# Kernel tuning notes

Hardware: AMD Instinct MI355X
Metric: run time of the kernel (lower is better)

## Reference

```python
import jax, jax.numpy as jnp
import numpy as np

NEG_SLOPE = 0.2
EPS = 1e-16


def _add_self_loops(edge_index, num_nodes):
    loop = jnp.arange(num_nodes, dtype=edge_index.dtype)
    return jnp.concatenate([edge_index, jnp.stack([loop, loop])], axis=1)


def gat_conv(x, edge_index, W, a_src, a_dst, b, concat):
    """PyG-style GATConv: gather -> attention logits -> segment softmax -> scatter-add."""
    N = x.shape[0]
    H, C = a_src.shape
    xl = (x @ W).reshape(N, H, C)                       # [N,H,C]
    alpha_src = (xl * a_src[None]).sum(-1)              # [N,H]
    alpha_dst = (xl * a_dst[None]).sum(-1)              # [N,H]
    src, dst = edge_index[0], edge_index[1]
    alpha = jax.nn.leaky_relu(alpha_src[src] + alpha_dst[dst], NEG_SLOPE)  # [E,H]
    amax = jax.ops.segment_max(alpha, dst, num_segments=N)
    amax = jnp.where(jnp.isfinite(amax), amax, 0.0)
    ea = jnp.exp(alpha - amax[dst])
    denom = jax.ops.segment_sum(ea, dst, num_segments=N)
    attn = ea / (denom[dst] + EPS)                      # [E,H]
    msg = xl[src] * attn[:, :, None]                    # [E,H,C]
    out = jax.ops.segment_sum(msg, dst, num_segments=N)  # [N,H,C]
    out = out.reshape(N, H * C) if concat else out.mean(axis=1)
    return out + b


def setup_inputs() -> dict:
    key = jax.random.key(0)
    ks = jax.random.split(key, 9)
    N, F, E, H, C, NC = 100000, 128, 1600000, 8, 8, 40
    s = lambda fan: 1.0 / np.sqrt(fan)
    return {
        "x": jax.random.normal(ks[0], (N, F), dtype=jnp.float32),
        "edge_index": jax.random.randint(ks[1], (2, E), 0, N, dtype=jnp.int64),
        "W1": jax.random.normal(ks[2], (F, H * C), dtype=jnp.float32) * s(F),
        "a_src1": jax.random.normal(ks[3], (H, C), dtype=jnp.float32) * s(C),
        "a_dst1": jax.random.normal(ks[4], (H, C), dtype=jnp.float32) * s(C),
        "b1": jnp.zeros((H * C,), dtype=jnp.float32),
        "W2": jax.random.normal(ks[5], (H * C, NC), dtype=jnp.float32) * s(H * C),
        "a_src2": jax.random.normal(ks[6], (1, NC), dtype=jnp.float32) * s(NC),
        "a_dst2": jax.random.normal(ks[7], (1, NC), dtype=jnp.float32) * s(NC),
        "b2": jnp.zeros((NC,), dtype=jnp.float32),
    }


def reference(x, edge_index, W1, a_src1, a_dst1, b1, W2, a_src2, a_dst2, b2):
    N = x.shape[0]
    ei = _add_self_loops(edge_index, N)
    h = gat_conv(x, ei, W1, a_src1, a_dst1, b1, concat=True)   # [N,64]
    h = jax.nn.elu(h)
    out = gat_conv(h, ei, W2, a_src2, a_dst2, b2, concat=True)  # [N,nclass]
    return out
```

## Files before the change

### kernel.cpp

```cpp
#include <hip/hip_runtime.h>
#include <math.h>

#define NEG_SLOPE 0.2f
#define GAT_EPS 1e-16f

#define CH   8192
#define NBK  256

__device__ __forceinline__ unsigned pack_bf16(float a, float b) {
    unsigned ua = __float_as_uint(a);
    unsigned ub = __float_as_uint(b);
    ua = (ua + 0x8000u) >> 16;
    ub = (ub + 0x8000u) & 0xffff0000u;
    return ua | ub;
}
__device__ __forceinline__ float bf_lo(unsigned pk) {
    return __uint_as_float(pk << 16);
}
__device__ __forceinline__ float bf_hi(unsigned pk) {
    return __uint_as_float(pk & 0xffff0000u);
}


__global__ __launch_bounds__(256) void k_cnt(
    const int* __restrict__ ei, int E, int N, int shift,
    int* __restrict__ cnt)
{
    __shared__ int h[NBK];
    int c = blockIdx.x;
    h[threadIdx.x] = 0;
    __syncthreads();
    int Etot = E + N;
    int base = c * CH;
    int lim = min(base + CH, Etot);
    for (int e = base + threadIdx.x; e < lim; e += 256) {
        int d = (e < E) ? ei[E + e] : (e - E);
        atomicAdd(&h[d >> shift], 1);
    }
    __syncthreads();
    cnt[c * NBK + threadIdx.x] = h[threadIdx.x];
}

__global__ __launch_bounds__(256) void k_off_a(
    const int* __restrict__ cnt, int* __restrict__ off,
    int* __restrict__ tot, int NCH)
{
    __shared__ int sm[256];
    int b = blockIdx.x;
    int t = threadIdx.x;
    int carry = 0;
    for (int c0 = 0; c0 < NCH; c0 += 256) {
        int c = c0 + t;
        int v = (c < NCH) ? cnt[c * NBK + b] : 0;
        sm[t] = v;
        __syncthreads();
        for (int o = 1; o < 256; o <<= 1) {
            int add = (t >= o) ? sm[t - o] : 0;
            __syncthreads();
            sm[t] += add;
            __syncthreads();
        }
        if (c < NCH) off[c * NBK + b] = carry + sm[t] - v;
        carry += sm[255];
        __syncthreads();
    }
    if (t == 0) tot[b] = carry;
}

__global__ __launch_bounds__(256) void k_off_b(
    const int* __restrict__ tot, int* __restrict__ bbase)
{
    __shared__ int sm[NBK];
    int b = threadIdx.x;
    int v0 = tot[b];
    sm[b] = v0;
    __syncthreads();
    for (int o = 1; o < NBK; o <<= 1) {
        int v = (b >= o) ? sm[b - o] : 0;
        __syncthreads();
        sm[b] += v;
        __syncthreads();
    }
    bbase[b] = sm[b] - v0;
    if (b == NBK - 1) bbase[NBK] = sm[b];
}

__global__ __launch_bounds__(256) void k_place(
    const int* __restrict__ ei, int E, int N, int shift,
    const int* __restrict__ off, const int* __restrict__ bbase,
    unsigned* __restrict__ bslab)
{
    __shared__ int cur[NBK];
    int c = blockIdx.x;
    cur[threadIdx.x] = bbase[threadIdx.x] + off[c * NBK + threadIdx.x];
    __syncthreads();
    int Etot = E + N;
    int base = c * CH;
    int lim = min(base + CH, Etot);
    int mask = (1 << shift) - 1;
    for (int e = base + threadIdx.x; e < lim; e += 256) {
        int s, d;
        if (e < E) { s = ei[e]; d = ei[E + e]; }
        else       { s = e - E; d = s; }
        int b = d >> shift;
        int pos = atomicAdd(&cur[b], 1);
        bslab[pos] = (unsigned)s | ((unsigned)(d & mask) << 17);
    }
}

__global__ __launch_bounds__(256) void k_csr2(
    const int* __restrict__ bbase, const unsigned* __restrict__ bslab,
    int shift, int* __restrict__ row_ptr, int* __restrict__ csr_src,
    int N, int Etot)
{
    __shared__ int sdeg[1024];
    __shared__ int scur[1024];
    __shared__ int ps[256];
    int b = blockIdx.x;
    int tid = threadIdx.x;
    int beg = bbase[b], end = bbase[b + 1];
    int nodes = 1 << shift;
    int node0 = b << shift;
    for (int i = tid; i < nodes; i += 256) sdeg[i] = 0;
    __syncthreads();
    for (int i = beg + tid; i < end; i += 256)
        atomicAdd(&sdeg[bslab[i] >> 17], 1);
    __syncthreads();
    int per = (nodes + 255) / 256;
    int mybase = tid * per;
    int sum = 0;
    for (int j = 0; j < per; j++) sum += sdeg[mybase + j];
    ps[tid] = sum;
    __syncthreads();
    int v0 = ps[tid];
    for (int o = 1; o < 256; o <<= 1) {
        int v = (tid >= o) ? ps[tid - o] : 0;
        __syncthreads();
        ps[tid] += v;
        __syncthreads();
    }
    int run = ps[tid] - v0;
    for (int j = 0; j < per; j++) {
        int i = mybase + j;
        int dgi = sdeg[i];
        scur[i] = beg + run;
        int node = node0 + i;
        if (node < N) row_ptr[node] = beg + run;
        run += dgi;
    }
    if (b == 0 && tid == 0) row_ptr[N] = Etot;
    __syncthreads();
    for (int i = beg + tid; i < end; i += 256) {
        unsigned w = bslab[i];
        int pos = atomicAdd(&scur[w >> 17], 1);
        csr_src[pos] = (int)(w & 0x1FFFFu);
    }
}

__global__ __launch_bounds__(256) void k_gemm1(
    const float* __restrict__ x, const float* __restrict__ W1,
    const float* __restrict__ a_src1, const float* __restrict__ a_dst1,
    unsigned* __restrict__ xl1b, float* __restrict__ as1,
    float* __restrict__ ad1, int N, int F)
{
    __shared__ float Ws[128 * 64];
    __shared__ float asrc[64];
    __shared__ float adst[64];
    for (int i = threadIdx.x; i < F * 64; i += 256) Ws[i] = W1[i];
    if (threadIdx.x < 64) {
        asrc[threadIdx.x] = a_src1[threadIdx.x];
        adst[threadIdx.x] = a_dst1[threadIdx.x];
    }
    __syncthreads();

    int n = blockIdx.x * 64 + (threadIdx.x >> 2);
    int q = threadIdx.x & 3;
    if (n >= N) return;
    int c0 = q * 16;

    float acc[16];
#pragma unroll
    for (int c = 0; c < 16; c++) acc[c] = 0.0f;

    const float4* xr4 = (const float4*)(x + (size_t)n * F);
    for (int k4 = 0; k4 < F / 4; k4++) {
        float4 xv = xr4[k4];
        const float* w0 = &Ws[(k4 * 4 + 0) * 64 + c0];
        const float* w1 = &Ws[(k4 * 4 + 1) * 64 + c0];
        const float* w2 = &Ws[(k4 * 4 + 2) * 64 + c0];
        const float* w3 = &Ws[(k4 * 4 + 3) * 64 + c0];
#pragma unroll
        for (int c = 0; c < 16; c++) {
            float a = acc[c];
            a = fmaf(xv.x, w0[c], a);
            a = fmaf(xv.y, w1[c], a);
            a = fmaf(xv.z, w2[c], a);
            a = fmaf(xv.w, w3[c], a);
            acc[c] = a;
        }
    }

    uint4 pk0, pk1;
    pk0.x = pack_bf16(acc[0], acc[1]);  pk0.y = pack_bf16(acc[2], acc[3]);
    pk0.z = pack_bf16(acc[4], acc[5]);  pk0.w = pack_bf16(acc[6], acc[7]);
    pk1.x = pack_bf16(acc[8], acc[9]);  pk1.y = pack_bf16(acc[10], acc[11]);
    pk1.z = pack_bf16(acc[12], acc[13]); pk1.w = pack_bf16(acc[14], acc[15]);
    uint4* xo = (uint4*)(xl1b + (size_t)n * 32 + q * 8);
    xo[0] = pk0;
    xo[1] = pk1;

#pragma unroll
    for (int hh = 0; hh < 2; hh++) {
        float s = 0.0f, t = 0.0f;
#pragma unroll
        for (int c = 0; c < 8; c++) {
            s = fmaf(acc[hh * 8 + c], asrc[c0 + hh * 8 + c], s);
            t = fmaf(acc[hh * 8 + c], adst[c0 + hh * 8 + c], t);
        }
        as1[(size_t)n * 8 + 2 * q + hh] = s;
        ad1[(size_t)n * 8 + 2 * q + hh] = t;
    }
}

__global__ __launch_bounds__(256) void k_agg1(
    const int* __restrict__ row_ptr, const int* __restrict__ csr_src,
    const float* __restrict__ as1, const float* __restrict__ ad1,
    const unsigned* __restrict__ xl1b, const float* __restrict__ b1,
    float* __restrict__ h1, int N)
{
    int d = blockIdx.x * 4 + (threadIdx.x >> 6);
    int lane = threadIdx.x & 63;
    if (d >= N) return;
    int g = lane >> 3;
    int l = lane & 7;

    int beg = row_ptr[d], end = row_ptr[d + 1];
    float adh = ad1[(size_t)d * 8 + l];

    float ax[8];
#pragma unroll
    for (int j = 0; j < 8; j++) ax[j] = 0.f;
    float den = 0.f;

    int i = beg + g;
    for (; i + 8 < end; i += 16) {
        int s0 = csr_src[i];
        int s1 = csr_src[i + 8];
        float al0 = as1[(size_t)s0 * 8 + l] + adh;
        float al1 = as1[(size_t)s1 * 8 + l] + adh;
        uint4 k0 = *(const uint4*)(xl1b + (size_t)s0 * 32 + l * 4);
        uint4 k1 = *(const uint4*)(xl1b + (size_t)s1 * 32 + l * 4);
        al0 = al0 > 0.f ? al0 : NEG_SLOPE * al0;
        al1 = al1 > 0.f ? al1 : NEG_SLOPE * al1;
        float e0 = __expf(al0);
        float e1 = __expf(al1);
        ax[0] = fmaf(e0, bf_lo(k0.x), ax[0]);
        ax[1] = fmaf(e0, bf_hi(k0.x), ax[1]);
        ax[2] = fmaf(e0, bf_lo(k0.y), ax[2]);
        ax[3] = fmaf(e0, bf_hi(k0.y), ax[3]);
        ax[4] = fmaf(e0, bf_lo(k0.z), ax[4]);
        ax[5] = fmaf(e0, bf_hi(k0.z), ax[5]);
        ax[6] = fmaf(e0, bf_lo(k0.w), ax[6]);
        ax[7] = fmaf(e0, bf_hi(k0.w), ax[7]);
        ax[0] = fmaf(e1, bf_lo(k1.x), ax[0]);
        ax[1] = fmaf(e1, bf_hi(k1.x), ax[1]);
        ax[2] = fmaf(e1, bf_lo(k1.y), ax[2]);
        ax[3] = fmaf(e1, bf_hi(k1.y), ax[3]);
        ax[4] = fmaf(e1, bf_lo(k1.z), ax[4]);
        ax[5] = fmaf(e1, bf_hi(k1.z), ax[5]);
        ax[6] = fmaf(e1, bf_lo(k1.w), ax[6]);
        ax[7] = fmaf(e1, bf_hi(k1.w), ax[7]);
        den += e0 + e1;
    }
    if (i < end) {
        int s0 = csr_src[i];
        float al0 = as1[(size_t)s0 * 8 + l] + adh;
        uint4 k0 = *(const uint4*)(xl1b + (size_t)s0 * 32 + l * 4);
        al0 = al0 > 0.f ? al0 : NEG_SLOPE * al0;
        float e0 = __expf(al0);
        ax[0] = fmaf(e0, bf_lo(k0.x), ax[0]);
        ax[1] = fmaf(e0, bf_hi(k0.x), ax[1]);
        ax[2] = fmaf(e0, bf_lo(k0.y), ax[2]);
        ax[3] = fmaf(e0, bf_hi(k0.y), ax[3]);
        ax[4] = fmaf(e0, bf_lo(k0.z), ax[4]);
        ax[5] = fmaf(e0, bf_hi(k0.z), ax[5]);
        ax[6] = fmaf(e0, bf_lo(k0.w), ax[6]);
        ax[7] = fmaf(e0, bf_hi(k0.w), ax[7]);
        den += e0;
    }

#pragma unroll
    for (int m = 8; m < 64; m <<= 1) {
#pragma unroll
        for (int j = 0; j < 8; j++) ax[j] += __shfl_xor(ax[j], m);
        den += __shfl_xor(den, m);
    }

    if (g == 0) {
        float inv = 1.f / (den + GAT_EPS);
        const float4* bb = (const float4*)(b1 + l * 8);
        float4 b0 = bb[0], b1v = bb[1];
        float4 o0, o1;
        float v;
        v = ax[0] * inv + b0.x; o0.x = v > 0.f ? v : expm1f(v);
        v = ax[1] * inv + b0.y; o0.y = v > 0.f ? v : expm1f(v);
        v = ax[2] * inv + b0.z; o0.z = v > 0.f ? v : expm1f(v);
        v = ax[3] * inv + b0.w; o0.w = v > 0.f ? v : expm1f(v);
        v = ax[4] * inv + b1v.x; o1.x = v > 0.f ? v : expm1f(v);
        v = ax[5] * inv + b1v.y; o1.y = v > 0.f ? v : expm1f(v);
        v = ax[6] * inv + b1v.z; o1.z = v > 0.f ? v : expm1f(v);
        v = ax[7] * inv + b1v.w; o1.w = v > 0.f ? v : expm1f(v);
        float4* op = (float4*)(h1 + (size_t)d * 64 + l * 8);
        op[0] = o0;
        op[1] = o1;
    }
}

__global__ __launch_bounds__(256) void k_node2(
    const float* __restrict__ h1, const float* __restrict__ W2,
    const float* __restrict__ a_src2, const float* __restrict__ a_dst2,
    unsigned* __restrict__ xl2b, float* __restrict__ as2,
    float* __restrict__ ad2, int N)
{
    __shared__ float Ws[64 * 40];
    __shared__ float a2s[40];
    __shared__ float a2d[40];
    for (int i = threadIdx.x; i < 64 * 40; i += 256) Ws[i] = W2[i];
    if (threadIdx.x < 40) {
        a2s[threadIdx.x] = a_src2[threadIdx.x];
        a2d[threadIdx.x] = a_dst2[threadIdx.x];
    }
    __syncthreads();

    int n = blockIdx.x * 128 + (threadIdx.x >> 1);
    int q = threadIdx.x & 1;
    if (n >= N) return;
    int c0 = q * 20;

    float o[20];
#pragma unroll
    for (int j = 0; j < 20; j++) o[j] = 0.0f;

    const float4* hr4 = (const float4*)(h1 + (size_t)n * 64);
    for (int k4 = 0; k4 < 16; k4++) {
        float4 hv = hr4[k4];
        const float* w0 = &Ws[(k4 * 4 + 0) * 40 + c0];
        const float* w1 = &Ws[(k4 * 4 + 1) * 40 + c0];
        const float* w2 = &Ws[(k4 * 4 + 2) * 40 + c0];
        const float* w3 = &Ws[(k4 * 4 + 3) * 40 + c0];
#pragma unroll
        for (int j = 0; j < 20; j++) {
            float a = o[j];
            a = fmaf(hv.x, w0[j], a);
            a = fmaf(hv.y, w1[j], a);
            a = fmaf(hv.z, w2[j], a);
            a = fmaf(hv.w, w3[j], a);
            o[j] = a;
        }
    }

    float s = 0.0f, t = 0.0f;
#pragma unroll
    for (int j = 0; j < 20; j++) {
        s = fmaf(o[j], a2s[c0 + j], s);
        t = fmaf(o[j], a2d[c0 + j], t);
    }
    s += __shfl_xor(s, 1);
    t += __shfl_xor(t, 1);
    if (q == 0) { as2[n] = s; ad2[n] = t; }

    unsigned* xo = xl2b + (size_t)n * 20 + q * 10;
#pragma unroll
    for (int p = 0; p < 10; p++) xo[p] = pack_bf16(o[2 * p], o[2 * p + 1]);
}

__global__ __launch_bounds__(256) void k_agg2(
    const int* __restrict__ row_ptr, const int* __restrict__ csr_src,
    const float* __restrict__ as2, const float* __restrict__ ad2,
    const unsigned* __restrict__ xl2b, const float* __restrict__ b2,
    float* __restrict__ out, int N)
{
    int d = blockIdx.x * 4 + (threadIdx.x >> 6);
    int lane = threadIdx.x & 63;
    if (d >= N) return;
    int g = lane >> 3;
    int l = lane & 7;
    if (l >= 5) return;

    int beg = row_ptr[d], end = row_ptr[d + 1];
    float add = ad2[d];

    float ax[8];
#pragma unroll
    for (int j = 0; j < 8; j++) ax[j] = 0.f;
    float den = 0.f;

    int i = beg + g;
    for (; i + 8 < end; i += 16) {
        int s0 = csr_src[i];
        int s1 = csr_src[i + 8];
        float al0 = as2[s0] + add;
        float al1 = as2[s1] + add;
        uint4 k0 = *(const uint4*)(xl2b + (size_t)s0 * 20 + l * 4);
        uint4 k1 = *(const uint4*)(xl2b + (size_t)s1 * 20 + l * 4);
        al0 = al0 > 0.f ? al0 : NEG_SLOPE * al0;
        al1 = al1 > 0.f ? al1 : NEG_SLOPE * al1;
        float e0 = __expf(al0);
        float e1 = __expf(al1);
        ax[0] = fmaf(e0, bf_lo(k0.x), ax[0]);
        ax[1] = fmaf(e0, bf_hi(k0.x), ax[1]);
        ax[2] = fmaf(e0, bf_lo(k0.y), ax[2]);
        ax[3] = fmaf(e0, bf_hi(k0.y), ax[3]);
        ax[4] = fmaf(e0, bf_lo(k0.z), ax[4]);
        ax[5] = fmaf(e0, bf_hi(k0.z), ax[5]);
        ax[6] = fmaf(e0, bf_lo(k0.w), ax[6]);
        ax[7] = fmaf(e0, bf_hi(k0.w), ax[7]);
        ax[0] = fmaf(e1, bf_lo(k1.x), ax[0]);
        ax[1] = fmaf(e1, bf_hi(k1.x), ax[1]);
        ax[2] = fmaf(e1, bf_lo(k1.y), ax[2]);
        ax[3] = fmaf(e1, bf_hi(k1.y), ax[3]);
        ax[4] = fmaf(e1, bf_lo(k1.z), ax[4]);
        ax[5] = fmaf(e1, bf_hi(k1.z), ax[5]);
        ax[6] = fmaf(e1, bf_lo(k1.w), ax[6]);
        ax[7] = fmaf(e1, bf_hi(k1.w), ax[7]);
        den += e0 + e1;
    }
    if (i < end) {
        int s0 = csr_src[i];
        float al0 = as2[s0] + add;
        uint4 k0 = *(const uint4*)(xl2b + (size_t)s0 * 20 + l * 4);
        al0 = al0 > 0.f ? al0 : NEG_SLOPE * al0;
        float e0 = __expf(al0);
        ax[0] = fmaf(e0, bf_lo(k0.x), ax[0]);
        ax[1] = fmaf(e0, bf_hi(k0.x), ax[1]);
        ax[2] = fmaf(e0, bf_lo(k0.y), ax[2]);
        ax[3] = fmaf(e0, bf_hi(k0.y), ax[3]);
        ax[4] = fmaf(e0, bf_lo(k0.z), ax[4]);
        ax[5] = fmaf(e0, bf_hi(k0.z), ax[5]);
        ax[6] = fmaf(e0, bf_lo(k0.w), ax[6]);
        ax[7] = fmaf(e0, bf_hi(k0.w), ax[7]);
        den += e0;
    }

#pragma unroll
    for (int m = 8; m < 64; m <<= 1) {
#pragma unroll
        for (int j = 0; j < 8; j++) ax[j] += __shfl_xor(ax[j], m);
        den += __shfl_xor(den, m);
    }

    if (g == 0) {
        float inv = 1.f / (den + GAT_EPS);
        float* op = out + (size_t)d * 40 + l * 8;
        const float* bb = b2 + l * 8;
#pragma unroll
        for (int j = 0; j < 8; j++) op[j] = ax[j] * inv + bb[j];
    }
}

extern "C" void kernel_launch(void* const* d_in, const int* in_sizes, int n_in,
                              void* d_out, int out_size, void* d_ws, size_t ws_size,
                              hipStream_t stream) {
    const float* x      = (const float*)d_in[0];
    const int*   ei     = (const int*)d_in[1];
    const float* W1     = (const float*)d_in[2];
    const float* a_src1 = (const float*)d_in[3];
    const float* a_dst1 = (const float*)d_in[4];
    const float* b1     = (const float*)d_in[5];
    const float* W2     = (const float*)d_in[6];
    const float* a_src2 = (const float*)d_in[7];
    const float* a_dst2 = (const float*)d_in[8];
    const float* b2     = (const float*)d_in[9];

    int F = in_sizes[2] / 64;
    int N = in_sizes[0] / F;
    int E = in_sizes[1] / 2;
    int Etot = E + N;
    int NCH = (Etot + CH - 1) / CH;
    int shift = 9;
    while (((N - 1) >> shift) >= NBK) shift++;

    unsigned* xl1b    = (unsigned*)d_ws;
    float*    h1      = (float*)(xl1b + (size_t)N * 32);
    float*    as1     = h1 + (size_t)N * 64;
    float*    ad1     = as1 + (size_t)N * 8;
    int*      row_ptr = (int*)(ad1 + (size_t)N * 8);
    int*      csr_src = row_ptr + (N + 1);
    int*      cnt     = csr_src + Etot;
    int*      off     = cnt + (size_t)NCH * NBK;
    int*      tot     = off + (size_t)NCH * NBK;
    int*      bbase   = tot + NBK;
    unsigned* bslab   = (unsigned*)(bbase + NBK + 1);
    unsigned* xl2b    = xl1b;
    float*    as2     = as1;
    float*    ad2     = ad1;

    k_cnt  <<<NCH, 256, 0, stream>>>(ei, E, N, shift, cnt);
    k_off_a<<<NBK, 256, 0, stream>>>(cnt, off, tot, NCH);
    k_off_b<<<1, 256, 0, stream>>>(tot, bbase);
    k_place<<<NCH, 256, 0, stream>>>(ei, E, N, shift, off, bbase, bslab);
    k_csr2 <<<NBK, 256, 0, stream>>>(bbase, bslab, shift,
                                     row_ptr, csr_src, N, Etot);

    k_gemm1<<<(N + 63) / 64, 256, 0, stream>>>(x, W1, a_src1, a_dst1,
                                               xl1b, as1, ad1, N, F);
    k_agg1 <<<(N + 3) / 4, 256, 0, stream>>>(row_ptr, csr_src, as1, ad1,
                                             xl1b, b1, h1, N);

    k_node2<<<(N + 127) / 128, 256, 0, stream>>>(h1, W2, a_src2, a_dst2,
                                                 xl2b, as2, ad2, N);
    k_agg2 <<<(N + 3) / 4, 256, 0, stream>>>(row_ptr, csr_src, as2, ad2,
                                             xl2b, b2, (float*)d_out, N);
}
```

Measured before the change: 315.1 us.

## Use half-wave per destination node and exp2-based attention with prescaled logits

The aggregation kernels now give each destination node 32 lanes instead of a full 64-lane wave, so each wave handles two nodes and per-node loop trip counts better match the average degree of about 17 edges. Attention logits are prescaled by log2(e) when written, which lets the edge loop use the hardware exp2 and a fmax-based leaky ReLU. The final division uses a hardware reciprocal, and the ELU uses fast exp instead of expm1f. The cost is a little precision in the softmax normalisation and in the ELU near zero, plus two edge streams per wave that may have different lengths and so diverge.

Measured after the change: 299.1 us. -5.1%, faster.

```diff
diff --git a/kernel.cpp b/kernel.cpp
--- a/kernel.cpp
+++ b/kernel.cpp
@@ -3,6 +3,7 @@
 
 #define NEG_SLOPE 0.2f
 #define GAT_EPS 1e-16f
+#define LOG2E 1.44269504088896340736f
 
 #define CH   8192
 #define NBK  256
@@ -217,8 +218,8 @@
             s = fmaf(acc[hh * 8 + c], asrc[c0 + hh * 8 + c], s);
             t = fmaf(acc[hh * 8 + c], adst[c0 + hh * 8 + c], t);
         }
-        as1[(size_t)n * 8 + 2 * q + hh] = s;
-        ad1[(size_t)n * 8 + 2 * q + hh] = t;
+        as1[(size_t)n * 8 + 2 * q + hh] = s * LOG2E;
+        ad1[(size_t)n * 8 + 2 * q + hh] = t * LOG2E;
     }
 }
 
@@ -228,9 +229,9 @@
     const unsigned* __restrict__ xl1b, const float* __restrict__ b1,
     float* __restrict__ h1, int N)
 {
-    int d = blockIdx.x * 4 + (threadIdx.x >> 6);
-    int lane = threadIdx.x & 63;
+    int d = blockIdx.x * 8 + ((threadIdx.x >> 6) << 1) + ((threadIdx.x >> 5) & 1);
     if (d >= N) return;
+    int lane = threadIdx.x & 31;
     int g = lane >> 3;
     int l = lane & 7;
 
@@ -243,17 +244,19 @@
     float den = 0.f;
 
     int i = beg + g;
-    for (; i + 8 < end; i += 16) {
+    for (; i + 4 < end; i += 8) {
         int s0 = csr_src[i];
-        int s1 = csr_src[i + 8];
-        float al0 = as1[(size_t)s0 * 8 + l] + adh;
-        float al1 = as1[(size_t)s1 * 8 + l] + adh;
-        uint4 k0 = *(const uint4*)(xl1b + (size_t)s0 * 32 + l * 4);
-        uint4 k1 = *(const uint4*)(xl1b + (size_t)s1 * 32 + l * 4);
-        al0 = al0 > 0.f ? al0 : NEG_SLOPE * al0;
-        al1 = al1 > 0.f ? al1 : NEG_SLOPE * al1;
-        float e0 = __expf(al0);
-        float e1 = __expf(al1);
+        int s1 = csr_src[i + 4];
+        size_t q0 = (size_t)s0 * 8 + l;
+        size_t q1 = (size_t)s1 * 8 + l;
+        float al0 = as1[q0] + adh;
+        float al1 = as1[q1] + adh;
+        uint4 k0 = *(const uint4*)(xl1b + (q0 << 2));
+        uint4 k1 = *(const uint4*)(xl1b + (q1 << 2));
+        al0 = fmaxf(al0, NEG_SLOPE * al0);
+        al1 = fmaxf(al1, NEG_SLOPE * al1);
+        float e0 = __builtin_amdgcn_exp2f(al0);
+        float e1 = __builtin_amdgcn_exp2f(al1);
         ax[0] = fmaf(e0, bf_lo(k0.x), ax[0]);
         ax[1] = fmaf(e0, bf_hi(k0.x), ax[1]);
         ax[2] = fmaf(e0, bf_lo(k0.y), ax[2]);
@@ -274,10 +277,11 @@
     }
     if (i < end) {
         int s0 = csr_src[i];
-        float al0 = as1[(size_t)s0 * 8 + l] + adh;
-        uint4 k0 = *(const uint4*)(xl1b + (size_t)s0 * 32 + l * 4);
-        al0 = al0 > 0.f ? al0 : NEG_SLOPE * al0;
-        float e0 = __expf(al0);
+        size_t q0 = (size_t)s0 * 8 + l;
+        float al0 = as1[q0] + adh;
+        uint4 k0 = *(const uint4*)(xl1b + (q0 << 2));
+        al0 = fmaxf(al0, NEG_SLOPE * al0);
+        float e0 = __builtin_amdgcn_exp2f(al0);
         ax[0] = fmaf(e0, bf_lo(k0.x), ax[0]);
         ax[1] = fmaf(e0, bf_hi(k0.x), ax[1]);
         ax[2] = fmaf(e0, bf_lo(k0.y), ax[2]);
@@ -290,26 +294,26 @@
     }
 
 #pragma unroll
-    for (int m = 8; m < 64; m <<= 1) {
+    for (int m = 8; m < 32; m <<= 1) {
 #pragma unroll
         for (int j = 0; j < 8; j++) ax[j] += __shfl_xor(ax[j], m);
         den += __shfl_xor(den, m);
     }
 
     if (g == 0) {
-        float inv = 1.f / (den + GAT_EPS);
+        float inv = __builtin_amdgcn_rcpf(den + GAT_EPS);
         const float4* bb = (const float4*)(b1 + l * 8);
         float4 b0 = bb[0], b1v = bb[1];
         float4 o0, o1;
         float v;
-        v = ax[0] * inv + b0.x; o0.x = v > 0.f ? v : expm1f(v);
-        v = ax[1] * inv + b0.y; o0.y = v > 0.f ? v : expm1f(v);
-        v = ax[2] * inv + b0.z; o0.z = v > 0.f ? v : expm1f(v);
-        v = ax[3] * inv + b0.w; o0.w = v > 0.f ? v : expm1f(v);
-        v = ax[4] * inv + b1v.x; o1.x = v > 0.f ? v : expm1f(v);
-        v = ax[5] * inv + b1v.y; o1.y = v > 0.f ? v : expm1f(v);
-        v = ax[6] * inv + b1v.z; o1.z = v > 0.f ? v : expm1f(v);
-        v = ax[7] * inv + b1v.w; o1.w = v > 0.f ? v : expm1f(v);
+        v = fmaf(ax[0], inv, b0.x);  o0.x = v > 0.f ? v : __expf(v) - 1.f;
+        v = fmaf(ax[1], inv, b0.y);  o0.y = v > 0.f ? v : __expf(v) - 1.f;
+        v = fmaf(ax[2], inv, b0.z);  o0.z = v > 0.f ? v : __expf(v) - 1.f;
+        v = fmaf(ax[3], inv, b0.w);  o0.w = v > 0.f ? v : __expf(v) - 1.f;
+        v = fmaf(ax[4], inv, b1v.x); o1.x = v > 0.f ? v : __expf(v) - 1.f;
+        v = fmaf(ax[5], inv, b1v.y); o1.y = v > 0.f ? v : __expf(v) - 1.f;
+        v = fmaf(ax[6], inv, b1v.z); o1.z = v > 0.f ? v : __expf(v) - 1.f;
+        v = fmaf(ax[7], inv, b1v.w); o1.w = v > 0.f ? v : __expf(v) - 1.f;
         float4* op = (float4*)(h1 + (size_t)d * 64 + l * 8);
         op[0] = o0;
         op[1] = o1;
@@ -367,7 +371,7 @@
     }
     s += __shfl_xor(s, 1);
     t += __shfl_xor(t, 1);
-    if (q == 0) { as2[n] = s; ad2[n] = t; }
+    if (q == 0) { as2[n] = s * LOG2E; ad2[n] = t * LOG2E; }
 
     unsigned* xo = xl2b + (size_t)n * 20 + q * 10;
 #pragma unroll
@@ -380,9 +384,9 @@
     const unsigned* __restrict__ xl2b, const float* __restrict__ b2,
     float* __restrict__ out, int N)
 {
-    int d = blockIdx.x * 4 + (threadIdx.x >> 6);
-    int lane = threadIdx.x & 63;
+    int d = blockIdx.x * 8 + ((threadIdx.x >> 6) << 1) + ((threadIdx.x >> 5) & 1);
     if (d >= N) return;
+    int lane = threadIdx.x & 31;
     int g = lane >> 3;
     int l = lane & 7;
     if (l >= 5) return;
@@ -396,17 +400,17 @@
     float den = 0.f;
 
     int i = beg + g;
-    for (; i + 8 < end; i += 16) {
+    for (; i + 4 < end; i += 8) {
         int s0 = csr_src[i];
-        int s1 = csr_src[i + 8];
+        int s1 = csr_src[i + 4];
         float al0 = as2[s0] + add;
         float al1 = as2[s1] + add;
         uint4 k0 = *(const uint4*)(xl2b + (size_t)s0 * 20 + l * 4);
         uint4 k1 = *(const uint4*)(xl2b + (size_t)s1 * 20 + l * 4);
-        al0 = al0 > 0.f ? al0 : NEG_SLOPE * al0;
-        al1 = al1 > 0.f ? al1 : NEG_SLOPE * al1;
-        float e0 = __expf(al0);
-        float e1 = __expf(al1);
+        al0 = fmaxf(al0, NEG_SLOPE * al0);
+        al1 = fmaxf(al1, NEG_SLOPE * al1);
+        float e0 = __builtin_amdgcn_exp2f(al0);
+        float e1 = __builtin_amdgcn_exp2f(al1);
         ax[0] = fmaf(e0, bf_lo(k0.x), ax[0]);
         ax[1] = fmaf(e0, bf_hi(k0.x), ax[1]);
         ax[2] = fmaf(e0, bf_lo(k0.y), ax[2]);
@@ -429,8 +433,8 @@
         int s0 = csr_src[i];
         float al0 = as2[s0] + add;
         uint4 k0 = *(const uint4*)(xl2b + (size_t)s0 * 20 + l * 4);
-        al0 = al0 > 0.f ? al0 : NEG_SLOPE * al0;
-        float e0 = __expf(al0);
+        al0 = fmaxf(al0, NEG_SLOPE * al0);
+        float e0 = __builtin_amdgcn_exp2f(al0);
         ax[0] = fmaf(e0, bf_lo(k0.x), ax[0]);
         ax[1] = fmaf(e0, bf_hi(k0.x), ax[1]);
         ax[2] = fmaf(e0, bf_lo(k0.y), ax[2]);
@@ -443,18 +447,18 @@
     }
 
 #pragma unroll
-    for (int m = 8; m < 64; m <<= 1) {
+    for (int m = 8; m < 32; m <<= 1) {
 #pragma unroll
         for (int j = 0; j < 8; j++) ax[j] += __shfl_xor(ax[j], m);
         den += __shfl_xor(den, m);
     }
 
     if (g == 0) {
-        float inv = 1.f / (den + GAT_EPS);
+        float inv = __builtin_amdgcn_rcpf(den + GAT_EPS);
         float* op = out + (size_t)d * 40 + l * 8;
         const float* bb = b2 + l * 8;
 #pragma unroll
-        for (int j = 0; j < 8; j++) op[j] = ax[j] * inv + bb[j];
+        for (int j = 0; j < 8; j++) op[j] = fmaf(ax[j], inv, bb[j]);
     }
 }
 
@@ -504,11 +508,11 @@
 
     k_gemm1<<<(N + 63) / 64, 256, 0, stream>>>(x, W1, a_src1, a_dst1,
                                                xl1b, as1, ad1, N, F);
-    k_agg1 <<<(N + 3) / 4, 256, 0, stream>>>(row_ptr, csr_src, as1, ad1,
+    k_agg1 <<<(N + 7) / 8, 256, 0, stream>>>(row_ptr, csr_src, as1, ad1,
                                              xl1b, b1, h1, N);
 
     k_node2<<<(N + 127) / 128, 256, 0, stream>>>(h1, W2, a_src2, a_dst2,
                                                  xl2b, as2, ad2, N);
-    k_agg2 <<<(N + 3) / 4, 256, 0, stream>>>(row_ptr, csr_src, as2, ad2,
+    k_agg2 <<<(N + 7) / 8, 256, 0, stream>>>(row_ptr, csr_src, as2, ad2,
                                              xl2b, b2, (float*)d_out, N);
 }
```
